# Kernel optimization log

Hardware: AMD Instinct MI355X
Metric: run time of the kernel (lower is better)

The kernel has to match this reference:

```python
import jax, jax.numpy as jnp
import numpy as np

B, S, D = 256, 70, 128
NUM_NODE = 40000
N_SAMPLE = 12
ALPHA = 0.2  # leaky-relu slope


def setup_inputs() -> dict:
    key = jax.random.key(0)
    ks = jax.random.split(key, 16)
    stdv = 1.0 / np.sqrt(D)
    u = lambda k, shp: jax.random.uniform(k, shp, jnp.float32, -stdv, stdv)
    inputs = jax.random.randint(ks[0], (B, S), 0, NUM_NODE)
    adj = jax.random.randint(ks[1], (B, S, S), 0, 5)
    mask_item = jnp.ones((B, S), jnp.int32)
    item = jax.random.randint(ks[2], (B, S), 0, NUM_NODE)
    input_times = jax.random.uniform(ks[3], (B, S), jnp.float32)
    adj_all = jax.random.randint(ks[4], (NUM_NODE, N_SAMPLE), 0, NUM_NODE)
    num_w = jax.random.uniform(ks[5], (NUM_NODE, N_SAMPLE), jnp.float32)
    embedding = u(ks[6], (NUM_NODE, D))
    a0, a1, a2, a3 = (u(ks[7 + i], (D,)) for i in range(4))
    gw1 = u(ks[11], (D + 1, D))
    gw2 = u(ks[12], (D, 1))
    gw3 = u(ks[13], (2 * D, D))
    gbias = u(ks[14], (D,))
    return dict(inputs=inputs, adj=adj, mask_item=mask_item, item=item,
                input_times=input_times, adj_all=adj_all, num_w=num_w,
                embedding=embedding, a0=a0, a1=a1, a2=a2, a3=a3,
                gw1=gw1, gw2=gw2, gw3=gw3, gbias=gbias)


def reference(inputs, adj, mask_item, item, input_times, adj_all, num_w,
              embedding, a0, a1, a2, a3, gw1, gw2, gw3, gbias):
    # ---- local aggregator (4-relation GAT over session graph) ----
    h = embedding[inputs]                              # [B,S,D]
    a_in = h[:, :, None, :] * h[:, None, :, :]         # [B,S,S,D] pairwise products
    att = lambda a: jax.nn.leaky_relu(jnp.einsum('bijd,d->bij', a_in, a), ALPHA)
    e0, e1, e2, e3 = att(a0), att(a1), att(a2), att(a3)
    neg = jnp.full_like(e0, -9e15)
    alpha = jnp.where(adj == 1, e0, neg)
    alpha = jnp.where(adj == 2, e1, alpha)
    alpha = jnp.where(adj == 3, e2, alpha)
    alpha = jnp.where(adj == 4, e3, alpha)
    alpha = jax.nn.softmax(alpha, axis=-1)
    h_local = jnp.einsum('bij,bjd->bid', alpha, h)     # [B,S,D]

    # ---- global aggregator: 1-hop neighbor sampling + session-gated attention ----
    flat = inputs.reshape(-1)
    neigh = adj_all[flat].reshape(B, S, N_SAMPLE)      # sampled neighbor ids
    nw = num_w[flat].reshape(B, S, N_SAMPLE)           # neighbor co-occurrence weights
    nv = embedding[neigh]                              # [B,S,K,D]

    maskf = mask_item.astype(jnp.float32)[..., None]   # [B,S,1]
    item_emb = embedding[item] * maskf
    sess = jnp.sum(item_emb, axis=1) / jnp.sum(maskf, axis=1)   # [B,D] mean session emb
    extra = sess[:, None, None, :]                     # broadcast to [B,S,K,D]

    feat = jnp.concatenate([extra * nv, nw[..., None]], axis=-1)  # [B,S,K,D+1]
    al = jax.nn.leaky_relu(feat @ gw1, 0.2)            # [B,S,K,D]
    al = jax.nn.softmax((al @ gw2)[..., 0], axis=-1)[..., None]   # [B,S,K,1]
    nagg = jnp.sum(al * nv, axis=-2)                   # [B,S,D]

    out = jnp.concatenate([h, nagg], axis=-1) @ gw3 + gbias
    h_global = jax.nn.relu(out)                        # [B,S,D]
    # dropout_local/global = 0 (eval mode): identity
    return h_local, h_global
```

## Files before the change

kernel.cpp:

```cpp
#include <hip/hip_runtime.h>
#include <hip/hip_bf16.h>

#define B_ 256
#define S_ 70
#define D_ 128
#define NSAMP 12
#define HGLOB (B_ * S_ * D_)
#define IBLK 14
#define NPOS 10
#define NR2 (NPOS * NSAMP)
#define NRP 128

typedef float  f32x4 __attribute__((ext_vector_type(4)));
typedef short  s16x8 __attribute__((ext_vector_type(8)));

__device__ __forceinline__ unsigned short f2bf(float x) {
    union { float f; unsigned u; } v; v.f = x;
    return (unsigned short)((v.u + 0x7FFF + ((v.u >> 16) & 1)) >> 16);
}
__device__ __forceinline__ float bf2f(unsigned short u) {
    union { unsigned u; float f; } v; v.u = ((unsigned)u) << 16;
    return v.f;
}

__global__ __launch_bounds__(512) void sess_kernel(const int* __restrict__ item,
                                                   const int* __restrict__ mask,
                                                   const float* __restrict__ emb,
                                                   float* __restrict__ sess) {
    __shared__ float pacc[4][D_];
    __shared__ float pm[4];
    int b = blockIdx.x;
    int d = threadIdx.x & 127, q = threadIdx.x >> 7;
    float acc = 0.f, msum = 0.f;
    for (int s = q; s < S_; s += 4) {
        int node = item[b * S_ + s];
        float m = (float)mask[b * S_ + s];
        acc += m * emb[(long)node * D_ + d];
        msum += m;
    }
    pacc[q][d] = acc;
    if (d == 0) pm[q] = msum;
    __syncthreads();
    if (q == 0) {
        float a = pacc[0][d] + pacc[1][d] + pacc[2][d] + pacc[3][d];
        float m = pm[0] + pm[1] + pm[2] + pm[3];
        sess[b * D_ + d] = a / m;
    }
}

__global__ __launch_bounds__(256) void pack_weights(const float* __restrict__ gw1,
                                                    const float* __restrict__ gw3,
                                                    unsigned short* __restrict__ gw1T,
                                                    unsigned short* __restrict__ gw3T) {
    int idx = blockIdx.x * 256 + threadIdx.x;
    if (idx < 128 * 128) {
        int c = idx >> 7, r = idx & 127;
        gw1T[idx] = f2bf(gw1[r * 128 + c]);
    }
    if (idx < 128 * 256) {
        int c = idx >> 8, r = idx & 255;
        gw3T[idx] = f2bf(gw3[r * 128 + c]);
    }
}

struct LocalSM {
    unsigned short hl[72 * 128];
    float          El[16 * 84];
    unsigned short al[16 * 104];
    int            ids[72];
};
struct GlobalSM {
    unsigned short nv[NRP * 128];
    unsigned short cat[16 * 256];
    float          spart[NRP][4];
    int            neigh[NR2];
    float          nw[NR2];
    float          score[NR2];
    float          wsm[NR2];
};

__global__ __launch_bounds__(256) void fused_kernel(
        const int* __restrict__ inputs, const int* __restrict__ adj,
        const int* __restrict__ adj_all, const float* __restrict__ num_w,
        const float* __restrict__ emb, const float* __restrict__ sess,
        const float* __restrict__ a0p, const float* __restrict__ a1p,
        const float* __restrict__ a2p, const float* __restrict__ a3p,
        const unsigned short* __restrict__ gw1T, const float* __restrict__ gw1,
        const float* __restrict__ gw2,
        const unsigned short* __restrict__ gw3T, const float* __restrict__ gbias,
        float* __restrict__ out) {
    __shared__ __align__(16) char smem[sizeof(GlobalSM)];

    const int L = blockIdx.x;
    const int b = L / 12;
    const int r = L - b * 12;
    const int tid  = threadIdx.x;
    const int lane = tid & 63, wave = tid >> 6;
    const int l15  = lane & 15, l4 = lane >> 4;
    const s16x8 zero8 = {0, 0, 0, 0, 0, 0, 0, 0};

    if (r < 5) {
        LocalSM* P = (LocalSM*)smem;
        const int i0 = r * IBLK;

        if (tid < S_) P->ids[tid] = inputs[b * S_ + tid];
        if (tid < 32) ((s16x8*)P->hl)[70 * 16 + tid] = zero8;
        __syncthreads();

        #pragma unroll
        for (int it = 0; it < 5; ++it) {
            int idx = it * 256 + tid;
            if (idx < S_ * 16) {
                int s = idx >> 4, c8 = idx & 15;
                const float4* ev = (const float4*)(emb + (long)P->ids[s] * D_ + c8 * 8);
                float4 e0 = ev[0], e1 = ev[1];
                s16x8 p;
                p[0] = (short)f2bf(e0.x); p[1] = (short)f2bf(e0.y);
                p[2] = (short)f2bf(e0.z); p[3] = (short)f2bf(e0.w);
                p[4] = (short)f2bf(e1.x); p[5] = (short)f2bf(e1.y);
                p[6] = (short)f2bf(e1.z); p[7] = (short)f2bf(e1.w);
                ((s16x8*)P->hl)[s * 16 + (c8 ^ (s & 7))] = p;
            }
        }
        __syncthreads();

        s16x8 af_all[4][4];
        {
            const float* aptr[4] = {a0p, a1p, a2p, a3p};
            int hrow = i0 + l15;
            #pragma unroll
            for (int ks = 0; ks < 4; ++ks) {
                s16x8 hf = ((s16x8*)P->hl)[hrow * 16 + ((ks * 4 + l4) ^ (hrow & 7))];
                #pragma unroll
                for (int rr = 0; rr < 4; ++rr) {
                    const float* ar = aptr[rr];
                    float4 alo = *(const float4*)(ar + ks * 32 + l4 * 8);
                    float4 ahi = *(const float4*)(ar + ks * 32 + l4 * 8 + 4);
                    s16x8 o;
                    o[0] = (short)f2bf(bf2f((unsigned short)hf[0]) * alo.x);
                    o[1] = (short)f2bf(bf2f((unsigned short)hf[1]) * alo.y);
                    o[2] = (short)f2bf(bf2f((unsigned short)hf[2]) * alo.z);
                    o[3] = (short)f2bf(bf2f((unsigned short)hf[3]) * alo.w);
                    o[4] = (short)f2bf(bf2f((unsigned short)hf[4]) * ahi.x);
                    o[5] = (short)f2bf(bf2f((unsigned short)hf[5]) * ahi.y);
                    o[6] = (short)f2bf(bf2f((unsigned short)hf[6]) * ahi.z);
                    o[7] = (short)f2bf(bf2f((unsigned short)hf[7]) * ahi.w);
                    af_all[rr][ks] = o;
                }
            }
        }

        for (int n = wave; n < 5; n += 4) {
            s16x8 bfr[4];
            int jr = n * 16 + l15;
            int jrc = jr < 72 ? jr : 71;
            #pragma unroll
            for (int ks = 0; ks < 4; ++ks)
                bfr[ks] = ((s16x8*)P->hl)[jrc * 16 + ((ks * 4 + l4) ^ (jrc & 7))];

            f32x4 ac0 = {0.f,0.f,0.f,0.f}, ac1 = {0.f,0.f,0.f,0.f};
            f32x4 ac2 = {0.f,0.f,0.f,0.f}, ac3 = {0.f,0.f,0.f,0.f};
            #pragma unroll
            for (int ks = 0; ks < 4; ++ks) {
                ac0 = __builtin_amdgcn_mfma_f32_16x16x32_bf16(af_all[0][ks], bfr[ks], ac0, 0, 0, 0);
                ac1 = __builtin_amdgcn_mfma_f32_16x16x32_bf16(af_all[1][ks], bfr[ks], ac1, 0, 0, 0);
                ac2 = __builtin_amdgcn_mfma_f32_16x16x32_bf16(af_all[2][ks], bfr[ks], ac2, 0, 0, 0);
                ac3 = __builtin_amdgcn_mfma_f32_16x16x32_bf16(af_all[3][ks], bfr[ks], ac3, 0, 0, 0);
            }

            #pragma unroll
            for (int reg = 0; reg < 4; ++reg) {
                int il = l4 * 4 + reg;
                int i  = i0 + il;
                int j  = n * 16 + l15;
                float v;
                if (j < S_) {
                    int ic = i < S_ ? i : S_ - 1;
                    int a  = adj[((long)b * S_ + ic) * S_ + j];
                    float raw = (a == 1) ? ac0[reg] : (a == 2) ? ac1[reg]
                              : (a == 3) ? ac2[reg] : (a == 4) ? ac3[reg] : 0.f;
                    v = (a >= 1 && a <= 4) ? (raw > 0.f ? raw : 0.2f * raw) : -9e15f;
                } else {
                    v = -INFINITY;
                }
                P->El[il * 84 + j] = v;
            }
        }
        __syncthreads();

        {
            int g = tid >> 4, li = tid & 15;
            float mx = -INFINITY;
            for (int j = li; j < S_; j += 16) mx = fmaxf(mx, P->El[g * 84 + j]);
            #pragma unroll
            for (int o = 1; o < 16; o <<= 1) mx = fmaxf(mx, __shfl_xor(mx, o));
            float sm = 0.f;
            for (int j = li; j < S_; j += 16) {
                float ex = __expf(P->El[g * 84 + j] - mx);
                P->El[g * 84 + j] = ex;
                sm += ex;
            }
            #pragma unroll
            for (int o = 1; o < 16; o <<= 1) sm += __shfl_xor(sm, o);
            float inv = 1.f / sm;
            for (int j = li; j < 104; j += 16)
                P->al[g * 104 + j] = (j < S_) ? f2bf(P->El[g * 84 + j] * inv) : (unsigned short)0;
        }
        __syncthreads();

        for (int n = wave; n < 8; n += 4) {
            f32x4 acc = {0.f, 0.f, 0.f, 0.f};
            int d = n * 16 + l15;
            int dchunk = d >> 3, de = d & 7;
            #pragma unroll
            for (int ks = 0; ks < 3; ++ks) {
                s16x8 afp = *(const s16x8*)(P->al + l15 * 104 + ks * 32 + l4 * 8);
                int jb = ks * 32 + l4 * 8;
                s16x8 bfp;
                #pragma unroll
                for (int e = 0; e < 8; ++e) {
                    int j = jb + e;
                    bfp[e] = (j < 72)
                        ? (short)P->hl[j * 128 + ((dchunk ^ (j & 7)) << 3) + de]
                        : (short)0;
                }
                acc = __builtin_amdgcn_mfma_f32_16x16x32_bf16(afp, bfp, acc, 0, 0, 0);
            }
            #pragma unroll
            for (int reg = 0; reg < 4; ++reg) {
                int il = l4 * 4 + reg;
                if (il < IBLK)
                    out[((long)b * S_ + (i0 + il)) * D_ + d] = acc[reg];
            }
        }
    } else {
        GlobalSM* P = (GlobalSM*)smem;
        const int i0  = (r - 5) * NPOS;
        const int bs0 = b * S_ + i0;

        if (tid < NR2) {
            int p = tid / NSAMP;
            int k = tid - p * NSAMP;
            int node = inputs[bs0 + p];
            P->neigh[tid] = adj_all[node * NSAMP + k];
            P->nw[tid]    = num_w[node * NSAMP + k];
        }
        if (tid < 128) ((s16x8*)P->nv)[NR2 * 16 + tid] = zero8;
        __syncthreads();

        #pragma unroll
        for (int it = 0; it < 8; ++it) {
            int idx = it * 256 + tid;
            if (idx < NR2 * 16) {
                int row = idx >> 4, c8 = idx & 15;
                const float4* ev = (const float4*)(emb + (long)P->neigh[row] * D_ + c8 * 8);
                float4 e0 = ev[0], e1 = ev[1];
                s16x8 p;
                p[0] = (short)f2bf(e0.x); p[1] = (short)f2bf(e0.y);
                p[2] = (short)f2bf(e0.z); p[3] = (short)f2bf(e0.w);
                p[4] = (short)f2bf(e1.x); p[5] = (short)f2bf(e1.y);
                p[6] = (short)f2bf(e1.z); p[7] = (short)f2bf(e1.w);
                ((s16x8*)P->nv)[row * 16 + (c8 ^ (row & 7))] = p;
            }
        }
        __syncthreads();

        s16x8 bfp[2][4];
        #pragma unroll
        for (int n = 0; n < 2; ++n) {
            int c = (wave * 2 + n) * 16 + l15;
            #pragma unroll
            for (int ks = 0; ks < 4; ++ks) {
                s16x8 g = *(const s16x8*)(gw1T + c * 128 + ks * 32 + l4 * 8);
                float4 slo = *(const float4*)(sess + b * D_ + ks * 32 + l4 * 8);
                float4 shi = *(const float4*)(sess + b * D_ + ks * 32 + l4 * 8 + 4);
                s16x8 o;
                o[0] = (short)f2bf(bf2f((unsigned short)g[0]) * slo.x);
                o[1] = (short)f2bf(bf2f((unsigned short)g[1]) * slo.y);
                o[2] = (short)f2bf(bf2f((unsigned short)g[2]) * slo.z);
                o[3] = (short)f2bf(bf2f((unsigned short)g[3]) * slo.w);
                o[4] = (short)f2bf(bf2f((unsigned short)g[4]) * shi.x);
                o[5] = (short)f2bf(bf2f((unsigned short)g[5]) * shi.y);
                o[6] = (short)f2bf(bf2f((unsigned short)g[6]) * shi.z);
                o[7] = (short)f2bf(bf2f((unsigned short)g[7]) * shi.w);
                bfp[n][ks] = o;
            }
        }
        float g128a = gw1[128 * 128 + wave * 32 + l15];
        float g128b = gw1[128 * 128 + wave * 32 + 16 + l15];
        float gw2a  = gw2[wave * 32 + l15];
        float gw2b  = gw2[wave * 32 + 16 + l15];

        for (int m = 0; m < NRP / 16; ++m) {
            int arow = m * 16 + l15;
            s16x8 af[4];
            #pragma unroll
            for (int ks = 0; ks < 4; ++ks)
                af[ks] = ((s16x8*)P->nv)[arow * 16 + ((ks * 4 + l4) ^ (arow & 7))];

            f32x4 acc0 = {0.f, 0.f, 0.f, 0.f}, acc1 = {0.f, 0.f, 0.f, 0.f};
            #pragma unroll
            for (int ks = 0; ks < 4; ++ks) {
                acc0 = __builtin_amdgcn_mfma_f32_16x16x32_bf16(af[ks], bfp[0][ks], acc0, 0, 0, 0);
                acc1 = __builtin_amdgcn_mfma_f32_16x16x32_bf16(af[ks], bfp[1][ks], acc1, 0, 0, 0);
            }

            float sp[4];
            #pragma unroll
            for (int reg = 0; reg < 4; ++reg) {
                int rr = m * 16 + l4 * 4 + reg;
                float nwv = (rr < NR2) ? P->nw[rr] : 0.f;
                float al0 = acc0[reg] + nwv * g128a;
                float al1 = acc1[reg] + nwv * g128b;
                al0 = al0 > 0.f ? al0 : 0.2f * al0;
                al1 = al1 > 0.f ? al1 : 0.2f * al1;
                sp[reg] = al0 * gw2a + al1 * gw2b;
            }
            #pragma unroll
            for (int off = 1; off < 16; off <<= 1) {
                #pragma unroll
                for (int reg = 0; reg < 4; ++reg) sp[reg] += __shfl_xor(sp[reg], off);
            }
            if (l15 == 0) {
                int rb = m * 16 + l4 * 4;
                #pragma unroll
                for (int reg = 0; reg < 4; ++reg) P->spart[rb + reg][wave] = sp[reg];
            }
        }
        __syncthreads();

        if (tid < NR2)
            P->score[tid] = P->spart[tid][0] + P->spart[tid][1] + P->spart[tid][2] + P->spart[tid][3];
        __syncthreads();

        if (tid < NPOS) {
            float mx = -1e30f;
            #pragma unroll
            for (int k = 0; k < NSAMP; ++k) mx = fmaxf(mx, P->score[tid * NSAMP + k]);
            float ex[NSAMP]; float ss = 0.f;
            #pragma unroll
            for (int k = 0; k < NSAMP; ++k) { ex[k] = __expf(P->score[tid * NSAMP + k] - mx); ss += ex[k]; }
            float inv = 1.f / ss;
            #pragma unroll
            for (int k = 0; k < NSAMP; ++k) P->wsm[tid * NSAMP + k] = ex[k] * inv;
        }
        __syncthreads();

        {
            int p  = tid >> 4;
            int c8 = tid & 15;
            if (p < NPOS) {
                float a0v[4] = {0.f,0.f,0.f,0.f}, a1v[4] = {0.f,0.f,0.f,0.f};
                #pragma unroll
                for (int k = 0; k < NSAMP; ++k) {
                    int row = p * NSAMP + k;
                    float w = P->wsm[row];
                    s16x8 nvv = ((s16x8*)P->nv)[row * 16 + (c8 ^ (row & 7))];
                    a0v[0] += w * bf2f((unsigned short)nvv[0]);
                    a0v[1] += w * bf2f((unsigned short)nvv[1]);
                    a0v[2] += w * bf2f((unsigned short)nvv[2]);
                    a0v[3] += w * bf2f((unsigned short)nvv[3]);
                    a1v[0] += w * bf2f((unsigned short)nvv[4]);
                    a1v[1] += w * bf2f((unsigned short)nvv[5]);
                    a1v[2] += w * bf2f((unsigned short)nvv[6]);
                    a1v[3] += w * bf2f((unsigned short)nvv[7]);
                }
                int node = inputs[bs0 + p];
                const float4* hv = (const float4*)(emb + (long)node * D_ + c8 * 8);
                float4 h0 = hv[0], h1 = hv[1];
                s16x8 ph, pa;
                ph[0]=(short)f2bf(h0.x); ph[1]=(short)f2bf(h0.y); ph[2]=(short)f2bf(h0.z); ph[3]=(short)f2bf(h0.w);
                ph[4]=(short)f2bf(h1.x); ph[5]=(short)f2bf(h1.y); ph[6]=(short)f2bf(h1.z); ph[7]=(short)f2bf(h1.w);
                pa[0]=(short)f2bf(a0v[0]); pa[1]=(short)f2bf(a0v[1]); pa[2]=(short)f2bf(a0v[2]); pa[3]=(short)f2bf(a0v[3]);
                pa[4]=(short)f2bf(a1v[0]); pa[5]=(short)f2bf(a1v[1]); pa[6]=(short)f2bf(a1v[2]); pa[7]=(short)f2bf(a1v[3]);
                ((s16x8*)P->cat)[p * 32 + ( c8       ^ (p & 7))] = ph;
                ((s16x8*)P->cat)[p * 32 + ((16 + c8) ^ (p & 7))] = pa;
            } else {
                ((s16x8*)P->cat)[p * 32 + ( c8       ^ (p & 7))] = zero8;
                ((s16x8*)P->cat)[p * 32 + ((16 + c8) ^ (p & 7))] = zero8;
            }
        }
        __syncthreads();

        {
            f32x4 acc0 = {0.f,0.f,0.f,0.f}, acc1 = {0.f,0.f,0.f,0.f};
            int arow = l15;
            int cc = wave * 32 + l15;
            #pragma unroll
            for (int ks = 0; ks < 8; ++ks) {
                s16x8 a  = ((s16x8*)P->cat)[arow * 32 + ((ks * 4 + l4) ^ (arow & 7))];
                s16x8 b0 = *(const s16x8*)(gw3T +  cc       * 256 + ks * 32 + l4 * 8);
                s16x8 b1 = *(const s16x8*)(gw3T + (cc + 16) * 256 + ks * 32 + l4 * 8);
                acc0 = __builtin_amdgcn_mfma_f32_16x16x32_bf16(a, b0, acc0, 0, 0, 0);
                acc1 = __builtin_amdgcn_mfma_f32_16x16x32_bf16(a, b1, acc1, 0, 0, 0);
            }
            float gb0 = gbias[wave * 32 + l15];
            float gb1 = gbias[wave * 32 + 16 + l15];
            #pragma unroll
            for (int reg = 0; reg < 4; ++reg) {
                int il = l4 * 4 + reg;
                if (il < NPOS) {
                    long bs = bs0 + il;
                    float o0 = acc0[reg] + gb0;
                    float o1 = acc1[reg] + gb1;
                    out[(long)HGLOB + bs * D_ + wave * 32 + l15]      = o0 > 0.f ? o0 : 0.f;
                    out[(long)HGLOB + bs * D_ + wave * 32 + 16 + l15] = o1 > 0.f ? o1 : 0.f;
                }
            }
        }
    }
}

extern "C" void kernel_launch(void* const* d_in, const int* in_sizes, int n_in,
                              void* d_out, int out_size, void* d_ws, size_t ws_size,
                              hipStream_t stream) {
    const int*   inputs  = (const int*)  d_in[0];
    const int*   adj     = (const int*)  d_in[1];
    const int*   mask    = (const int*)  d_in[2];
    const int*   item    = (const int*)  d_in[3];
    const int*   adj_all = (const int*)  d_in[5];
    const float* num_w   = (const float*)d_in[6];
    const float* emb     = (const float*)d_in[7];
    const float* a0      = (const float*)d_in[8];
    const float* a1      = (const float*)d_in[9];
    const float* a2      = (const float*)d_in[10];
    const float* a3      = (const float*)d_in[11];
    const float* gw1     = (const float*)d_in[12];
    const float* gw2     = (const float*)d_in[13];
    const float* gw3     = (const float*)d_in[14];
    const float* gbias   = (const float*)d_in[15];
    float* out = (float*)d_out;

    float*          sess = (float*)d_ws;
    unsigned short* gw1T = (unsigned short*)((char*)d_ws + 131072);
    unsigned short* gw3T = gw1T + 128 * 128;

    sess_kernel<<<B_, 512, 0, stream>>>(item, mask, emb, sess);
    pack_weights<<<128, 256, 0, stream>>>(gw1, gw3, gw1T, gw3T);
    fused_kernel<<<B_ * 12, 256, 0, stream>>>(inputs, adj, adj_all, num_w, emb, sess,
                                              a0, a1, a2, a3,
                                              gw1T, gw1, gw2, gw3T, gbias, out);
}
```

Measured before the change: 83.98 us.

## Halve global-branch positions per block and merge prelude kernels into one launch

After: 125.8 us. +49.8%, slower.

```diff
diff --git a/kernel.cpp b/kernel.cpp
--- a/kernel.cpp
+++ b/kernel.cpp
@@ -7,9 +7,10 @@
 #define NSAMP 12
 #define HGLOB (B_ * S_ * D_)
 #define IBLK 14
-#define NPOS 10
+#define NPOS 5
 #define NR2 (NPOS * NSAMP)
-#define NRP 128
+#define NRP 64
+#define NROLE (5 + 14)
 
 typedef float  f32x4 __attribute__((ext_vector_type(4)));
 typedef short  s16x8 __attribute__((ext_vector_type(8)));
@@ -23,43 +24,44 @@
     return v.f;
 }
 
-__global__ __launch_bounds__(512) void sess_kernel(const int* __restrict__ item,
-                                                   const int* __restrict__ mask,
-                                                   const float* __restrict__ emb,
-                                                   float* __restrict__ sess) {
-    __shared__ float pacc[4][D_];
-    __shared__ float pm[4];
-    int b = blockIdx.x;
-    int d = threadIdx.x & 127, q = threadIdx.x >> 7;
-    float acc = 0.f, msum = 0.f;
-    for (int s = q; s < S_; s += 4) {
-        int node = item[b * S_ + s];
-        float m = (float)mask[b * S_ + s];
-        acc += m * emb[(long)node * D_ + d];
-        msum += m;
-    }
-    pacc[q][d] = acc;
-    if (d == 0) pm[q] = msum;
-    __syncthreads();
-    if (q == 0) {
-        float a = pacc[0][d] + pacc[1][d] + pacc[2][d] + pacc[3][d];
-        float m = pm[0] + pm[1] + pm[2] + pm[3];
-        sess[b * D_ + d] = a / m;
-    }
-}
-
-__global__ __launch_bounds__(256) void pack_weights(const float* __restrict__ gw1,
-                                                    const float* __restrict__ gw3,
-                                                    unsigned short* __restrict__ gw1T,
-                                                    unsigned short* __restrict__ gw3T) {
-    int idx = blockIdx.x * 256 + threadIdx.x;
-    if (idx < 128 * 128) {
-        int c = idx >> 7, r = idx & 127;
-        gw1T[idx] = f2bf(gw1[r * 128 + c]);
-    }
-    if (idx < 128 * 256) {
-        int c = idx >> 8, r = idx & 255;
-        gw3T[idx] = f2bf(gw3[r * 128 + c]);
+__global__ __launch_bounds__(512) void prelude_kernel(const int* __restrict__ item,
+                                                      const int* __restrict__ mask,
+                                                      const float* __restrict__ emb,
+                                                      const float* __restrict__ gw1,
+                                                      const float* __restrict__ gw3,
+                                                      float* __restrict__ sess,
+                                                      unsigned short* __restrict__ gw1T,
+                                                      unsigned short* __restrict__ gw3T) {
+    if (blockIdx.x < B_) {
+        __shared__ float pacc[4][D_];
+        __shared__ float pm[4];
+        int b = blockIdx.x;
+        int d = threadIdx.x & 127, q = threadIdx.x >> 7;
+        float acc = 0.f, msum = 0.f;
+        for (int s = q; s < S_; s += 4) {
+            int node = item[b * S_ + s];
+            float m = (float)mask[b * S_ + s];
+            acc += m * emb[(long)node * D_ + d];
+            msum += m;
+        }
+        pacc[q][d] = acc;
+        if (d == 0) pm[q] = msum;
+        __syncthreads();
+        if (q == 0) {
+            float a = pacc[0][d] + pacc[1][d] + pacc[2][d] + pacc[3][d];
+            float m = pm[0] + pm[1] + pm[2] + pm[3];
+            sess[b * D_ + d] = a / m;
+        }
+    } else {
+        int idx = (blockIdx.x - B_) * 512 + threadIdx.x;
+        if (idx < 128 * 128) {
+            int c = idx >> 7, r = idx & 127;
+            gw1T[idx] = f2bf(gw1[r * 128 + c]);
+        } else if (idx < 128 * 128 + 128 * 256) {
+            int j = idx - 128 * 128;
+            int c = j >> 8, r = j & 255;
+            gw3T[j] = f2bf(gw3[r * 128 + c]);
+        }
     }
 }
 
@@ -79,6 +81,8 @@
     float          wsm[NR2];
 };
 
+union FusedSM { LocalSM loc; GlobalSM glob; };
+
 __global__ __launch_bounds__(256) void fused_kernel(
         const int* __restrict__ inputs, const int* __restrict__ adj,
         const int* __restrict__ adj_all, const float* __restrict__ num_w,
@@ -89,18 +93,18 @@
         const float* __restrict__ gw2,
         const unsigned short* __restrict__ gw3T, const float* __restrict__ gbias,
         float* __restrict__ out) {
-    __shared__ __align__(16) char smem[sizeof(GlobalSM)];
+    __shared__ __align__(16) FusedSM smem;
 
     const int L = blockIdx.x;
-    const int b = L / 12;
-    const int r = L - b * 12;
+    const int b = L / NROLE;
+    const int r = L - b * NROLE;
     const int tid  = threadIdx.x;
     const int lane = tid & 63, wave = tid >> 6;
     const int l15  = lane & 15, l4 = lane >> 4;
     const s16x8 zero8 = {0, 0, 0, 0, 0, 0, 0, 0};
 
     if (r < 5) {
-        LocalSM* P = (LocalSM*)smem;
+        LocalSM* P = &smem.loc;
         const int i0 = r * IBLK;
 
         if (tid < S_) P->ids[tid] = inputs[b * S_ + tid];
@@ -234,7 +238,7 @@
             }
         }
     } else {
-        GlobalSM* P = (GlobalSM*)smem;
+        GlobalSM* P = &smem.glob;
         const int i0  = (r - 5) * NPOS;
         const int bs0 = b * S_ + i0;
 
@@ -245,11 +249,11 @@
             P->neigh[tid] = adj_all[node * NSAMP + k];
             P->nw[tid]    = num_w[node * NSAMP + k];
         }
-        if (tid < 128) ((s16x8*)P->nv)[NR2 * 16 + tid] = zero8;
+        if (tid < (NRP - NR2) * 16) ((s16x8*)P->nv)[NR2 * 16 + tid] = zero8;
         __syncthreads();
 
         #pragma unroll
-        for (int it = 0; it < 8; ++it) {
+        for (int it = 0; it < 4; ++it) {
             int idx = it * 256 + tid;
             if (idx < NR2 * 16) {
                 int row = idx >> 4, c8 = idx & 15;
@@ -435,9 +439,8 @@
     unsigned short* gw1T = (unsigned short*)((char*)d_ws + 131072);
     unsigned short* gw3T = gw1T + 128 * 128;
 
-    sess_kernel<<<B_, 512, 0, stream>>>(item, mask, emb, sess);
-    pack_weights<<<128, 256, 0, stream>>>(gw1, gw3, gw1T, gw3T);
-    fused_kernel<<<B_ * 12, 256, 0, stream>>>(inputs, adj, adj_all, num_w, emb, sess,
-                                              a0, a1, a2, a3,
-                                              gw1T, gw1, gw2, gw3T, gbias, out);
+    prelude_kernel<<<B_ + 96, 512, 0, stream>>>(item, mask, emb, gw1, gw3, sess, gw1T, gw3T);
+    fused_kernel<<<B_ * NROLE, 256, 0, stream>>>(inputs, adj, adj_all, num_w, emb, sess,
+                                                 a0, a1, a2, a3,
+                                                 gw1T, gw1, gw2, gw3T, gbias, out);
 }
```
